# Performance work log

Measured on AMD Instinct MI355X. Metric: run time of the kernel, lower is better.

## Reference

```python
import jax, jax.numpy as jnp
import numpy as np

NUM_HEADS = 16
SPAN = 256  # pos_ebd_size (position_buckets)


def _split_heads(x, num_heads):
    # x: (B, S, D) -> (B*num_heads, S, D//num_heads)
    b, s, d = x.shape
    return x.reshape(b, s, num_heads, d // num_heads).transpose(0, 2, 1, 3).reshape(b * num_heads, s, d // num_heads)


def setup_inputs() -> dict:
    key = jax.random.key(0)
    ks = jax.random.split(key, 12)
    B, S, D = 1, 2048, 1024
    std = 0.02
    n_src = NUM_HEADS * S * 2 * SPAN   # flat size of c2p/p2c score tensor
    n_dst = NUM_HEADS * S * S          # flat size of gathered bias
    return {
        "hidden_states": jax.random.normal(ks[0], (B, S, D), jnp.float32),
        "rel_embeddings": jax.random.normal(ks[1], (2 * SPAN, D), jnp.float32),
        "Wq": jax.random.normal(ks[2], (D, D), jnp.float32) * std,
        "bq": jnp.zeros((D,), jnp.float32),
        "Wk": jax.random.normal(ks[3], (D, D), jnp.float32) * std,
        "bk": jnp.zeros((D,), jnp.float32),
        "Wv": jax.random.normal(ks[4], (D, D), jnp.float32) * std,
        "bv": jnp.zeros((D,), jnp.float32),
        "ids": jax.random.randint(ks[5], (n_dst,), 0, n_src, jnp.int32),
        "ids_t": jax.random.randint(ks[6], (n_dst,), 0, n_src, jnp.int32),
    }


def reference(hidden_states, rel_embeddings, Wq, bq, Wk, bk, Wv, bv, ids, ids_t):
    B, S, D = hidden_states.shape
    dh = D // NUM_HEADS
    # pos_att_type = ['c2p','p2c'] -> scale_factor = 3
    scale = jnp.sqrt(jnp.asarray(dh * 3, jnp.float32))

    q = _split_heads(hidden_states @ Wq + bq, NUM_HEADS)  # (B*H, S, dh)
    k = _split_heads(hidden_states @ Wk + bk, NUM_HEADS)
    v = _split_heads(hidden_states @ Wv + bv, NUM_HEADS)

    scores = jnp.einsum('bsd,btd->bst', q, k) / scale  # (B*H, S, S)

    # share_att_key=True: reuse key/query projections on relative embeddings
    pos = rel_embeddings[: 2 * SPAN][None]             # (1, 2*SPAN, D)
    pos_k = _split_heads(pos @ Wk + bk, NUM_HEADS)     # (H, 2*SPAN, dh)
    pos_q = _split_heads(pos @ Wq + bq, NUM_HEADS)

    bs = q.shape[0]  # == H when B == 1 (required by the original bmm)
    # c2p: gather from flattened (bs, S, 2*SPAN) scores
    c2p = jnp.einsum('bsd,bkd->bsk', q, pos_k)
    c2p_bias = c2p.reshape(-1)[ids].reshape(bs, S, S) / scale
    # p2c: gather then transpose last two dims
    p2c = jnp.einsum('bsd,bkd->bsk', k, pos_q)
    p2c_bias = jnp.swapaxes(p2c.reshape(-1)[ids_t].reshape(bs, S, S), -1, -2) / scale

    scores = scores + c2p_bias + p2c_bias
    probs = jax.nn.softmax(scores, axis=-1)
    ctx = jnp.einsum('bst,btd->bsd', probs, v)         # (B*H, S, dh)
    ctx = ctx.reshape(B, NUM_HEADS, S, dh).transpose(0, 2, 1, 3).reshape(B, S, D)
    return ctx
```

## Files before the change

### kernel.cpp

```cpp
#include <hip/hip_runtime.h>
#include <math.h>

#define S_LEN 2048
#define D_DIM 1024
#define NH 16
#define DH 64
#define NPOS 512

__global__ __launch_bounds__(256) void proj_gemm(
    const float* __restrict__ X, const float* __restrict__ W,
    const float* __restrict__ bias, float* __restrict__ outp, int M) {
  __shared__ float xt[16][132];
  __shared__ float wt[16][128];
  const int tid = threadIdx.x;
  const int br = blockIdx.y, bc = blockIdx.x;
  const int r0 = (tid >> 4) * 8, c0 = (tid & 15) * 8;
  float acc[8][8];
  #pragma unroll
  for (int i = 0; i < 8; i++)
    #pragma unroll
    for (int j = 0; j < 8; j++) acc[i][j] = 0.f;

  const float* Xb = X + (size_t)br * 128 * D_DIM;
  const float* Wb = W + bc * 128;

  for (int k0 = 0; k0 < D_DIM; k0 += 16) {
    __syncthreads();
    #pragma unroll
    for (int i = 0; i < 2; i++) {
      int slot = tid + i * 256;
      int row = slot >> 2;
      int kc = (slot & 3) * 4;
      float4 xv = *(const float4*)(Xb + (size_t)row * D_DIM + k0 + kc);
      xt[kc + 0][row] = xv.x; xt[kc + 1][row] = xv.y;
      xt[kc + 2][row] = xv.z; xt[kc + 3][row] = xv.w;
      int kr = slot >> 5;
      int wc = (slot & 31) * 4;
      *(float4*)&wt[kr][wc] = *(const float4*)(Wb + (size_t)(k0 + kr) * D_DIM + wc);
    }
    __syncthreads();
    #pragma unroll
    for (int kk = 0; kk < 16; kk++) {
      float a[8], b[8];
      *(float4*)&a[0] = *(const float4*)&xt[kk][r0];
      *(float4*)&a[4] = *(const float4*)&xt[kk][r0 + 4];
      *(float4*)&b[0] = *(const float4*)&wt[kk][c0];
      *(float4*)&b[4] = *(const float4*)&wt[kk][c0 + 4];
      #pragma unroll
      for (int ii = 0; ii < 8; ii++)
        #pragma unroll
        for (int jj = 0; jj < 8; jj++)
          acc[ii][jj] = fmaf(a[ii], b[jj], acc[ii][jj]);
    }
  }

  const int n0 = bc * 128 + c0;
  const int h = n0 >> 6, iw = n0 & 63;
  float bvals[8];
  #pragma unroll
  for (int jj = 0; jj < 8; jj++) bvals[jj] = bias[n0 + jj];
  #pragma unroll
  for (int ii = 0; ii < 8; ii++) {
    size_t row = (size_t)br * 128 + r0 + ii;
    float ov[8];
    #pragma unroll
    for (int jj = 0; jj < 8; jj++) ov[jj] = acc[ii][jj] + bvals[jj];
    float* dst = outp + ((size_t)h * M + row) * 64 + iw;
    *(float4*)dst = *(float4*)&ov[0];
    *(float4*)(dst + 4) = *(float4*)&ov[4];
  }
}

__global__ __launch_bounds__(256) void rel_gemm(
    const float* __restrict__ q_ws, const float* __restrict__ k_ws,
    const float* __restrict__ pk_ws, const float* __restrict__ pq_ws,
    float* __restrict__ c2p, float* __restrict__ p2c, float inv_scale) {
  __shared__ float at[16][132];
  __shared__ float bt[16][132];
  const int tid = threadIdx.x;
  const int h = blockIdx.z & 15;
  const int which = blockIdx.z >> 4;
  const float* A = (which ? k_ws : q_ws) + (size_t)h * S_LEN * DH;
  const float* Bm = (which ? pq_ws : pk_ws) + (size_t)h * NPOS * DH;
  float* C = (which ? p2c : c2p) + (size_t)h * S_LEN * NPOS;
  const int br = blockIdx.y, bc = blockIdx.x;
  const int r0 = (tid >> 4) * 8, c0 = (tid & 15) * 8;
  float acc[8][8];
  #pragma unroll
  for (int i = 0; i < 8; i++)
    #pragma unroll
    for (int j = 0; j < 8; j++) acc[i][j] = 0.f;

  for (int k0 = 0; k0 < DH; k0 += 16) {
    __syncthreads();
    #pragma unroll
    for (int i = 0; i < 2; i++) {
      int slot = tid + i * 256;
      int row = slot >> 2;
      int kc = (slot & 3) * 4;
      float4 av = *(const float4*)(A + (size_t)(br * 128 + row) * DH + k0 + kc);
      at[kc + 0][row] = av.x; at[kc + 1][row] = av.y;
      at[kc + 2][row] = av.z; at[kc + 3][row] = av.w;
      float4 bv = *(const float4*)(Bm + (size_t)(bc * 128 + row) * DH + k0 + kc);
      bt[kc + 0][row] = bv.x; bt[kc + 1][row] = bv.y;
      bt[kc + 2][row] = bv.z; bt[kc + 3][row] = bv.w;
    }
    __syncthreads();
    #pragma unroll
    for (int kk = 0; kk < 16; kk++) {
      float a[8], b[8];
      *(float4*)&a[0] = *(const float4*)&at[kk][r0];
      *(float4*)&a[4] = *(const float4*)&at[kk][r0 + 4];
      *(float4*)&b[0] = *(const float4*)&bt[kk][c0];
      *(float4*)&b[4] = *(const float4*)&bt[kk][c0 + 4];
      #pragma unroll
      for (int ii = 0; ii < 8; ii++)
        #pragma unroll
        for (int jj = 0; jj < 8; jj++)
          acc[ii][jj] = fmaf(a[ii], b[jj], acc[ii][jj]);
    }
  }
  #pragma unroll
  for (int ii = 0; ii < 8; ii++) {
    size_t row = (size_t)br * 128 + r0 + ii;
    float ov[8];
    #pragma unroll
    for (int jj = 0; jj < 8; jj++) ov[jj] = acc[ii][jj] * inv_scale;
    float* dst = C + row * NPOS + bc * 128 + c0;
    *(float4*)dst = *(float4*)&ov[0];
    *(float4*)(dst + 4) = *(float4*)&ov[4];
  }
}

__global__ __launch_bounds__(256) void attn_kernel(
    const float* __restrict__ q_ws, const float* __restrict__ k_ws,
    const float* __restrict__ v_ws, const float* __restrict__ c2p,
    const float* __restrict__ p2c, const int* __restrict__ ids,
    const int* __restrict__ ids_t, float* __restrict__ outp, float inv_scale) {
  __shared__ float qT[64][68];
  __shared__ float kT[64][68];
  __shared__ float vS[64][64];
  const int tid = threadIdx.x;
  const int h = blockIdx.y;
  const int s0 = blockIdx.x * 64;
  const int r4 = tid >> 4, c4 = tid & 15;
  const int r0 = r4 * 4, c0 = c4 * 4;

  const float* qb = q_ws + ((size_t)h * S_LEN + s0) * DH;
  const float* kb = k_ws + (size_t)h * S_LEN * DH;
  const float* vb = v_ws + (size_t)h * S_LEN * DH;

  #pragma unroll
  for (int i = 0; i < 4; i++) {
    int slot = tid + i * 256;
    int s = slot >> 4;
    int dc = (slot & 15) * 4;
    float4 qv = *(const float4*)(qb + (size_t)s * DH + dc);
    qT[dc + 0][s] = qv.x; qT[dc + 1][s] = qv.y;
    qT[dc + 2][s] = qv.z; qT[dc + 3][s] = qv.w;
  }

  float m[4], l[4], o[4][4];
  #pragma unroll
  for (int ii = 0; ii < 4; ii++) {
    m[ii] = -INFINITY; l[ii] = 0.f;
    #pragma unroll
    for (int jj = 0; jj < 4; jj++) o[ii][jj] = 0.f;
  }

  for (int kt = 0; kt < S_LEN / 64; kt++) {
    const int t0 = kt * 64;
    __syncthreads();
    #pragma unroll
    for (int i = 0; i < 4; i++) {
      int slot = tid + i * 256;
      int t = slot >> 4;
      int dc = (slot & 15) * 4;
      float4 kv = *(const float4*)(kb + (size_t)(t0 + t) * DH + dc);
      kT[dc + 0][t] = kv.x; kT[dc + 1][t] = kv.y;
      kT[dc + 2][t] = kv.z; kT[dc + 3][t] = kv.w;
      float4 vv = *(const float4*)(vb + (size_t)(t0 + t) * DH + dc);
      *(float4*)&vS[t][dc] = vv;
    }
    __syncthreads();

    float sc[4][4];
    #pragma unroll
    for (int ii = 0; ii < 4; ii++)
      #pragma unroll
      for (int jj = 0; jj < 4; jj++) sc[ii][jj] = 0.f;
    #pragma unroll 8
    for (int d = 0; d < 64; d++) {
      float a[4], b[4];
      *(float4*)a = *(const float4*)&qT[d][r0];
      *(float4*)b = *(const float4*)&kT[d][c0];
      #pragma unroll
      for (int ii = 0; ii < 4; ii++)
        #pragma unroll
        for (int jj = 0; jj < 4; jj++)
          sc[ii][jj] = fmaf(a[ii], b[jj], sc[ii][jj]);
    }
    #pragma unroll
    for (int ii = 0; ii < 4; ii++)
      #pragma unroll
      for (int jj = 0; jj < 4; jj++) sc[ii][jj] *= inv_scale;

    #pragma unroll
    for (int ii = 0; ii < 4; ii++) {
      const size_t s = s0 + r0 + ii;
      int4 iv = *(const int4*)(ids + ((size_t)h * S_LEN + s) * S_LEN + t0 + c0);
      sc[ii][0] += c2p[iv.x]; sc[ii][1] += c2p[iv.y];
      sc[ii][2] += c2p[iv.z]; sc[ii][3] += c2p[iv.w];
    }
    #pragma unroll
    for (int jj = 0; jj < 4; jj++) {
      const size_t t = t0 + c0 + jj;
      int4 iv = *(const int4*)(ids_t + ((size_t)h * S_LEN + t) * S_LEN + s0 + r0);
      sc[0][jj] += p2c[iv.x]; sc[1][jj] += p2c[iv.y];
      sc[2][jj] += p2c[iv.z]; sc[3][jj] += p2c[iv.w];
    }

    #pragma unroll
    for (int ii = 0; ii < 4; ii++) {
      float v = fmaxf(fmaxf(sc[ii][0], sc[ii][1]), fmaxf(sc[ii][2], sc[ii][3]));
      v = fmaxf(v, __shfl_xor(v, 1));
      v = fmaxf(v, __shfl_xor(v, 2));
      v = fmaxf(v, __shfl_xor(v, 4));
      v = fmaxf(v, __shfl_xor(v, 8));
      float mn = fmaxf(m[ii], v);
      float alpha = __expf(m[ii] - mn);
      m[ii] = mn;
      float rs = 0.f;
      #pragma unroll
      for (int jj = 0; jj < 4; jj++) {
        sc[ii][jj] = __expf(sc[ii][jj] - mn);
        rs += sc[ii][jj];
      }
      rs += __shfl_xor(rs, 1);
      rs += __shfl_xor(rs, 2);
      rs += __shfl_xor(rs, 4);
      rs += __shfl_xor(rs, 8);
      l[ii] = l[ii] * alpha + rs;
      #pragma unroll
      for (int jj = 0; jj < 4; jj++) o[ii][jj] *= alpha;
    }

    __syncthreads();
    #pragma unroll
    for (int jj = 0; jj < 4; jj++) {
      float pv[4] = {sc[0][jj], sc[1][jj], sc[2][jj], sc[3][jj]};
      *(float4*)&kT[c0 + jj][r0] = *(float4*)pv;
    }
    __syncthreads();

    #pragma unroll 8
    for (int t = 0; t < 64; t++) {
      float a[4], b[4];
      *(float4*)a = *(const float4*)&kT[t][r0];
      *(float4*)b = *(const float4*)&vS[t][c0];
      #pragma unroll
      for (int ii = 0; ii < 4; ii++)
        #pragma unroll
        for (int jj = 0; jj < 4; jj++)
          o[ii][jj] = fmaf(a[ii], b[jj], o[ii][jj]);
    }
  }

  #pragma unroll
  for (int ii = 0; ii < 4; ii++) {
    float inv_l = 1.0f / l[ii];
    float ov[4];
    #pragma unroll
    for (int jj = 0; jj < 4; jj++) ov[jj] = o[ii][jj] * inv_l;
    float* dst = outp + (size_t)(s0 + r0 + ii) * D_DIM + h * DH + c0;
    *(float4*)dst = *(float4*)ov;
  }
}

extern "C" void kernel_launch(void* const* d_in, const int* in_sizes, int n_in,
                              void* d_out, int out_size, void* d_ws, size_t ws_size,
                              hipStream_t stream) {
  const float* hs  = (const float*)d_in[0];
  const float* rel = (const float*)d_in[1];
  const float* Wq  = (const float*)d_in[2];
  const float* bq  = (const float*)d_in[3];
  const float* Wk  = (const float*)d_in[4];
  const float* bk  = (const float*)d_in[5];
  const float* Wv  = (const float*)d_in[6];
  const float* bv  = (const float*)d_in[7];
  const int* ids   = (const int*)d_in[8];
  const int* ids_t = (const int*)d_in[9];
  float* outp = (float*)d_out;

  float* ws = (float*)d_ws;
  float* q_ws  = ws;
  float* k_ws  = q_ws + 2097152;
  float* v_ws  = k_ws + 2097152;
  float* pk_ws = v_ws + 2097152;
  float* pq_ws = pk_ws + 524288;
  float* c2p_ws = pq_ws + 524288;
  float* p2c_ws = c2p_ws + 16777216;

  const float inv_scale = 1.0f / sqrtf((float)(DH * 3));

  dim3 blk(256);
  proj_gemm<<<dim3(8, 16), blk, 0, stream>>>(hs, Wq, bq, q_ws, S_LEN);
  proj_gemm<<<dim3(8, 16), blk, 0, stream>>>(hs, Wk, bk, k_ws, S_LEN);
  proj_gemm<<<dim3(8, 16), blk, 0, stream>>>(hs, Wv, bv, v_ws, S_LEN);
  proj_gemm<<<dim3(8, 4),  blk, 0, stream>>>(rel, Wk, bk, pk_ws, NPOS);
  proj_gemm<<<dim3(8, 4),  blk, 0, stream>>>(rel, Wq, bq, pq_ws, NPOS);
  rel_gemm<<<dim3(4, 16, 32), blk, 0, stream>>>(q_ws, k_ws, pk_ws, pq_ws,
                                                c2p_ws, p2c_ws, inv_scale);
  attn_kernel<<<dim3(32, 16), blk, 0, stream>>>(q_ws, k_ws, v_ws, c2p_ws,
                                                p2c_ws, ids, ids_t, outp, inv_scale);
}
```

Baseline: 3.569 ms.

## Double attention block threads and prefetch gather indices one tile ahead

Raises the attention kernel to 512 threads per block, with each thread owning 2 query rows instead of 4, so more wavefronts are resident to hide the latency of the random c2p/p2c gathers. Index vectors for the next key tile are loaded with nontemporal loads during the current tile's compute. The K/V global loads and bias gathers are issued before the LDS barrier so they overlap synchronisation. Output stores become nontemporal and the barriers use an explicit lgkmcnt wait; the cost is more register-held prefetch state and smaller per-thread tiles, which lowers FMA reuse from LDS.

```diff
diff --git a/kernel.cpp b/kernel.cpp
--- a/kernel.cpp
+++ b/kernel.cpp
@@ -6,6 +6,16 @@
 #define NH 16
 #define DH 64
 #define NPOS 512
+#define NT (S_LEN / 64)
+
+typedef int   ivec4 __attribute__((ext_vector_type(4)));
+typedef int   ivec2 __attribute__((ext_vector_type(2)));
+typedef float fvec4 __attribute__((ext_vector_type(4)));
+
+__device__ __forceinline__ void bar_lgkm() {
+  asm volatile("s_waitcnt lgkmcnt(0)" ::: "memory");
+  __builtin_amdgcn_s_barrier();
+}
 
 __global__ __launch_bounds__(256) void proj_gemm(
     const float* __restrict__ X, const float* __restrict__ W,
@@ -132,7 +142,7 @@
   }
 }
 
-__global__ __launch_bounds__(256) void attn_kernel(
+__global__ __launch_bounds__(512, 4) void attn_kernel(
     const float* __restrict__ q_ws, const float* __restrict__ k_ws,
     const float* __restrict__ v_ws, const float* __restrict__ c2p,
     const float* __restrict__ p2c, const int* __restrict__ ids,
@@ -143,16 +153,20 @@
   const int tid = threadIdx.x;
   const int h = blockIdx.y;
   const int s0 = blockIdx.x * 64;
-  const int r4 = tid >> 4, c4 = tid & 15;
-  const int r0 = r4 * 4, c0 = c4 * 4;
+  const int r4 = tid >> 4;
+  const int c4 = tid & 15;
+  const int r0 = r4 * 2;
+  const int c0 = c4 * 4;
 
   const float* qb = q_ws + ((size_t)h * S_LEN + s0) * DH;
   const float* kb = k_ws + (size_t)h * S_LEN * DH;
   const float* vb = v_ws + (size_t)h * S_LEN * DH;
-
-  #pragma unroll
-  for (int i = 0; i < 4; i++) {
-    int slot = tid + i * 256;
+  const int* idc = ids   + (size_t)h * S_LEN * S_LEN;
+  const int* idp = ids_t + (size_t)h * S_LEN * S_LEN;
+
+  #pragma unroll
+  for (int i = 0; i < 2; i++) {
+    int slot = tid + i * 512;
     int s = slot >> 4;
     int dc = (slot & 15) * 4;
     float4 qv = *(const float4*)(qb + (size_t)s * DH + dc);
@@ -160,68 +174,96 @@
     qT[dc + 2][s] = qv.z; qT[dc + 3][s] = qv.w;
   }
 
-  float m[4], l[4], o[4][4];
-  #pragma unroll
-  for (int ii = 0; ii < 4; ii++) {
+  float m[2], l[2], o[2][4];
+  #pragma unroll
+  for (int ii = 0; ii < 2; ii++) {
     m[ii] = -INFINITY; l[ii] = 0.f;
     #pragma unroll
     for (int jj = 0; jj < 4; jj++) o[ii][jj] = 0.f;
   }
 
-  for (int kt = 0; kt < S_LEN / 64; kt++) {
+  ivec4 ia[2];
+  ivec2 ib[4];
+  #pragma unroll
+  for (int ii = 0; ii < 2; ii++)
+    ia[ii] = __builtin_nontemporal_load(
+        (const ivec4*)(idc + (size_t)(s0 + r0 + ii) * S_LEN + c0));
+  #pragma unroll
+  for (int jj = 0; jj < 4; jj++)
+    ib[jj] = __builtin_nontemporal_load(
+        (const ivec2*)(idp + (size_t)(c0 + jj) * S_LEN + s0 + r0));
+
+  for (int kt = 0; kt < NT; kt++) {
     const int t0 = kt * 64;
-    __syncthreads();
-    #pragma unroll
-    for (int i = 0; i < 4; i++) {
-      int slot = tid + i * 256;
-      int t = slot >> 4;
-      int dc = (slot & 15) * 4;
-      float4 kv = *(const float4*)(kb + (size_t)(t0 + t) * DH + dc);
-      kT[dc + 0][t] = kv.x; kT[dc + 1][t] = kv.y;
-      kT[dc + 2][t] = kv.z; kT[dc + 3][t] = kv.w;
-      float4 vv = *(const float4*)(vb + (size_t)(t0 + t) * DH + dc);
-      *(float4*)&vS[t][dc] = vv;
-    }
-    __syncthreads();
-
-    float sc[4][4];
-    #pragma unroll
-    for (int ii = 0; ii < 4; ii++)
+
+    float4 kreg[2], vreg[2];
+    int ts[2], dcs[2];
+    #pragma unroll
+    for (int i = 0; i < 2; i++) {
+      int slot = tid + i * 512;
+      ts[i] = slot >> 4;
+      dcs[i] = (slot & 15) * 4;
+      kreg[i] = *(const float4*)(kb + (size_t)(t0 + ts[i]) * DH + dcs[i]);
+      vreg[i] = *(const float4*)(vb + (size_t)(t0 + ts[i]) * DH + dcs[i]);
+    }
+
+    float gc[2][4], gp[4][2];
+    #pragma unroll
+    for (int ii = 0; ii < 2; ii++) {
+      gc[ii][0] = c2p[ia[ii][0]]; gc[ii][1] = c2p[ia[ii][1]];
+      gc[ii][2] = c2p[ia[ii][2]]; gc[ii][3] = c2p[ia[ii][3]];
+    }
+    #pragma unroll
+    for (int jj = 0; jj < 4; jj++) {
+      gp[jj][0] = p2c[ib[jj][0]];
+      gp[jj][1] = p2c[ib[jj][1]];
+    }
+
+    bar_lgkm();
+    #pragma unroll
+    for (int i = 0; i < 2; i++) {
+      kT[dcs[i] + 0][ts[i]] = kreg[i].x; kT[dcs[i] + 1][ts[i]] = kreg[i].y;
+      kT[dcs[i] + 2][ts[i]] = kreg[i].z; kT[dcs[i] + 3][ts[i]] = kreg[i].w;
+      *(float4*)&vS[ts[i]][dcs[i]] = vreg[i];
+    }
+    bar_lgkm();
+
+    float sc[2][4];
+    #pragma unroll
+    for (int ii = 0; ii < 2; ii++)
       #pragma unroll
       for (int jj = 0; jj < 4; jj++) sc[ii][jj] = 0.f;
     #pragma unroll 8
     for (int d = 0; d < 64; d++) {
-      float a[4], b[4];
-      *(float4*)a = *(const float4*)&qT[d][r0];
+      float a[2], b[4];
+      *(float2*)a = *(const float2*)&qT[d][r0];
       *(float4*)b = *(const float4*)&kT[d][c0];
       #pragma unroll
-      for (int ii = 0; ii < 4; ii++)
+      for (int ii = 0; ii < 2; ii++)
         #pragma unroll
         for (int jj = 0; jj < 4; jj++)
           sc[ii][jj] = fmaf(a[ii], b[jj], sc[ii][jj]);
     }
-    #pragma unroll
-    for (int ii = 0; ii < 4; ii++)
-      #pragma unroll
-      for (int jj = 0; jj < 4; jj++) sc[ii][jj] *= inv_scale;
-
-    #pragma unroll
-    for (int ii = 0; ii < 4; ii++) {
-      const size_t s = s0 + r0 + ii;
-      int4 iv = *(const int4*)(ids + ((size_t)h * S_LEN + s) * S_LEN + t0 + c0);
-      sc[ii][0] += c2p[iv.x]; sc[ii][1] += c2p[iv.y];
-      sc[ii][2] += c2p[iv.z]; sc[ii][3] += c2p[iv.w];
-    }
-    #pragma unroll
-    for (int jj = 0; jj < 4; jj++) {
-      const size_t t = t0 + c0 + jj;
-      int4 iv = *(const int4*)(ids_t + ((size_t)h * S_LEN + t) * S_LEN + s0 + r0);
-      sc[0][jj] += p2c[iv.x]; sc[1][jj] += p2c[iv.y];
-      sc[2][jj] += p2c[iv.z]; sc[3][jj] += p2c[iv.w];
-    }
-
-    #pragma unroll
-    for (int ii = 0; ii < 4; ii++) {
+
+    if (kt + 1 < NT) {
+      #pragma unroll
+      for (int ii = 0; ii < 2; ii++)
+        ia[ii] = __builtin_nontemporal_load(
+            (const ivec4*)(idc + (size_t)(s0 + r0 + ii) * S_LEN + t0 + 64 + c0));
+      #pragma unroll
+      for (int jj = 0; jj < 4; jj++)
+        ib[jj] = __builtin_nontemporal_load(
+            (const ivec2*)(idp + (size_t)(t0 + 64 + c0 + jj) * S_LEN + s0 + r0));
+    }
+
+    #pragma unroll
+    for (int ii = 0; ii < 2; ii++)
+      #pragma unroll
+      for (int jj = 0; jj < 4; jj++)
+        sc[ii][jj] = fmaf(sc[ii][jj], inv_scale, gc[ii][jj] + gp[jj][ii]);
+
+    #pragma unroll
+    for (int ii = 0; ii < 2; ii++) {
       float v = fmaxf(fmaxf(sc[ii][0], sc[ii][1]), fmaxf(sc[ii][2], sc[ii][3]));
       v = fmaxf(v, __shfl_xor(v, 1));
       v = fmaxf(v, __shfl_xor(v, 2));
@@ -245,21 +287,21 @@
       for (int jj = 0; jj < 4; jj++) o[ii][jj] *= alpha;
     }
 
-    __syncthreads();
+    bar_lgkm();
     #pragma unroll
     for (int jj = 0; jj < 4; jj++) {
-      float pv[4] = {sc[0][jj], sc[1][jj], sc[2][jj], sc[3][jj]};
-      *(float4*)&kT[c0 + jj][r0] = *(float4*)pv;
-    }
-    __syncthreads();
+      float pv[2] = {sc[0][jj], sc[1][jj]};
+      *(float2*)&kT[c0 + jj][r0] = *(float2*)pv;
+    }
+    bar_lgkm();
 
     #pragma unroll 8
     for (int t = 0; t < 64; t++) {
-      float a[4], b[4];
-      *(float4*)a = *(const float4*)&kT[t][r0];
+      float a[2], b[4];
+      *(float2*)a = *(const float2*)&kT[t][r0];
       *(float4*)b = *(const float4*)&vS[t][c0];
       #pragma unroll
-      for (int ii = 0; ii < 4; ii++)
+      for (int ii = 0; ii < 2; ii++)
         #pragma unroll
         for (int jj = 0; jj < 4; jj++)
           o[ii][jj] = fmaf(a[ii], b[jj], o[ii][jj]);
@@ -267,13 +309,13 @@
   }
 
   #pragma unroll
-  for (int ii = 0; ii < 4; ii++) {
+  for (int ii = 0; ii < 2; ii++) {
     float inv_l = 1.0f / l[ii];
-    float ov[4];
+    fvec4 ov;
     #pragma unroll
     for (int jj = 0; jj < 4; jj++) ov[jj] = o[ii][jj] * inv_l;
     float* dst = outp + (size_t)(s0 + r0 + ii) * D_DIM + h * DH + c0;
-    *(float4*)dst = *(float4*)ov;
+    __builtin_nontemporal_store(ov, (fvec4*)dst);
   }
 }
 
@@ -311,6 +353,6 @@
   proj_gemm<<<dim3(8, 4),  blk, 0, stream>>>(rel, Wq, bq, pq_ws, NPOS);
   rel_gemm<<<dim3(4, 16, 32), blk, 0, stream>>>(q_ws, k_ws, pk_ws, pq_ws,
                                                 c2p_ws, p2c_ws, inv_scale);
-  attn_kernel<<<dim3(32, 16), blk, 0, stream>>>(q_ws, k_ws, v_ws, c2p_ws,
-                                                p2c_ws, ids, ids_t, outp, inv_scale);
-}
+  attn_kernel<<<dim3(32, 16), dim3(512), 0, stream>>>(
+      q_ws, k_ws, v_ws, c2p_ws, p2c_ws, ids, ids_t, outp, inv_scale);
+}
```

Result: no change. 3.605 ms (+1.0%).
